# Optimization experiments

Hardware: AMD Instinct MI355X
Metric: run time of the kernel (lower is better)

The kernel has to match this reference:

```python
import jax, jax.numpy as jnp
import numpy as np
from jax import lax

K = 3          # kernel_size
G = 2          # num_groups
DN = ('NHWC', 'HWIO', 'NHWC')


def _conv_same(x, w, b, groups=1):
    y = lax.conv_general_dilated(x, w, (1, 1), 'SAME',
                                 dimension_numbers=DN,
                                 feature_group_count=groups)
    return y + b


def _kernel_grid():
    off = (K - 1) / 2.0
    lin = jnp.linspace(-off, off, K, dtype=jnp.float32)
    dx, dy = jnp.meshgrid(lin, lin)              # 'xy' indexing, like tf default
    return jnp.stack([dx, dy], axis=-1).reshape(K * K, 2)  # [K2, 2] (dx, dy)


def _bilinear_sample(inp, loc):
    # inp: [B,H,W,C], loc: [B,H,W,K2,2] with (x,y) already clipped to valid range
    B, H, W, C = inp.shape
    x, y = loc[..., 0], loc[..., 1]
    x0 = jnp.floor(x); y0 = jnp.floor(y)
    x1 = jnp.clip(x0 + 1.0, 0.0, W - 1.0); x0 = jnp.clip(x0, 0.0, W - 1.0)
    y1 = jnp.clip(y0 + 1.0, 0.0, H - 1.0); y0 = jnp.clip(y0, 0.0, H - 1.0)
    # corner weights (computed from clipped coords, matching the TF code)
    wa = (x1 - x) * (y1 - y)
    wb = (x1 - x) * (y - y0)
    wc = (x - x0) * (y1 - y)
    wd = (x - x0) * (y - y0)
    x0i = x0.astype(jnp.int32); x1i = x1.astype(jnp.int32)
    y0i = y0.astype(jnp.int32); y1i = y1.astype(jnp.int32)
    flat = inp.reshape(B, H * W, C)

    def gather(yi, xi):
        idx = (yi * W + xi).reshape(B, -1, 1)               # [B, H*W*K2, 1]
        v = jnp.take_along_axis(flat, idx, axis=1)          # [B, H*W*K2, C]
        return v.reshape(B, H, W, K * K, C)

    out = (wa[..., None] * gather(y0i, x0i) + wb[..., None] * gather(y1i, x0i)
           + wc[..., None] * gather(y0i, x1i) + wd[..., None] * gather(y1i, x1i))
    return out  # [B,H,W,K2,C]


def _forward(x, off_w, off_b, dw_w, dw_b, pw_w, pw_b):
    B, H, W, C = x.shape
    Cg = C // G
    kg = _kernel_grid()                                     # [K2,2]
    gx, gy = jnp.meshgrid(jnp.arange(W, dtype=jnp.float32),
                          jnp.arange(H, dtype=jnp.float32))
    grid = jnp.stack([gx, gy], axis=-1)                     # [H,W,2] (x,y)
    outs = []
    for g in range(G):
        xi = x[..., g * Cg:(g + 1) * Cg]                    # [B,H,W,Cg]
        offsets = _conv_same(xi, off_w[g], off_b[g])        # [B,H,W,2*K2]
        offsets = offsets.reshape(B, H, W, K * K, 2)
        loc = grid[None, :, :, None, :] + kg[None, None, None] + offsets
        loc = jnp.stack([jnp.clip(loc[..., 0], 0.0, W - 1.0),
                         jnp.clip(loc[..., 1], 0.0, H - 1.0)], axis=-1)
        sampled = _bilinear_sample(xi, loc)                 # [B,H,W,K2,Cg]
        Kin = K * K * Cg
        s = sampled.reshape(B, H, W, Kin)
        s = _conv_same(s, dw_w[g], dw_b[g], groups=Kin)     # depthwise 3x3
        s = _conv_same(s, pw_w[g], pw_b[g])                 # 1x1 pointwise
        outs.append(s)
    return jnp.concatenate(outs, axis=-1)


def setup_inputs() -> dict:
    key = jax.random.key(0)
    ks = jax.random.split(key, 6)
    B, H, W, C = 4, 128, 128, 128
    Cg = C // G
    F = 128
    Fg = F // G
    Kin = K * K * Cg
    x = jax.random.normal(ks[0], (B, H, W, C), jnp.float32)
    # offset conv (zero-init in source; small random weights so offsets ~1px)
    off_w = jax.random.normal(ks[1], (G, K, K, Cg, 2 * K * K), jnp.float32) * 0.05
    off_b = jnp.zeros((G, 2 * K * K), jnp.float32)
    dw_w = jax.random.normal(ks[2], (G, K, K, 1, Kin), jnp.float32) * 0.1
    dw_b = jnp.zeros((G, Kin), jnp.float32)
    pw_w = jax.random.normal(ks[3], (G, 1, 1, Kin, Fg), jnp.float32) / np.sqrt(Kin)
    pw_b = jnp.zeros((G, Fg), jnp.float32)
    return {"x": x, "off_w": off_w, "off_b": off_b,
            "dw_w": dw_w, "dw_b": dw_b, "pw_w": pw_w, "pw_b": pw_b}


def reference(x, off_w, off_b, dw_w, dw_b, pw_w, pw_b):
    return _forward(x, off_w, off_b, dw_w, dw_b, pw_w, pw_b)
```

## Files before the change

kernel.cpp:

```cpp
#include <hip/hip_runtime.h>
#include <hip/hip_bf16.h>

#define HW 128
#define GNUM 2
#define BATCH 4
#define OBT_STRIDE (GNUM * 18 * 2 * 512)
#define PWT_FLOATS 36864
#define OBT_FLOATS 36864

typedef short s16x8 __attribute__((ext_vector_type(8)));
typedef float f32x4 __attribute__((ext_vector_type(4)));

__device__ inline unsigned short f2bf(float f) {
    union { float f; unsigned u; } v;
    v.f = f;
    unsigned r = (v.u + 0x7fffu + ((v.u >> 16) & 1u)) >> 16;
    return (unsigned short)r;
}
__device__ inline unsigned pk2bf(float lo, float hi) {
    __hip_bfloat162 r = __float22bfloat162_rn(float2{lo, hi});
    return *(unsigned*)&r;
}
__device__ inline float blo(unsigned u) {
    union { unsigned u; float f; } v; v.u = u << 16; return v.f;
}
__device__ inline float bhi(unsigned u) {
    union { unsigned u; float f; } v; v.u = u & 0xffff0000u; return v.f;
}

__global__ __launch_bounds__(256) void prep_kernel(
    const float* __restrict__ pw_w, const float* __restrict__ dw_b,
    const float* __restrict__ off_w, unsigned short* __restrict__ pwt,
    unsigned short* __restrict__ obt, float* __restrict__ bias2) {
    const int g = blockIdx.y;
    const int t = threadIdx.x;
    if (blockIdx.x < 9) {
        const int j = blockIdx.x;
        const int wv = t >> 6, lane = t & 63;
        const int f = wv * 16 + (lane & 15);
        const int kbase = (lane >> 4) << 3;
        float part = 0.f;
#pragma unroll
        for (int ks = 0; ks < 2; ++ks)
#pragma unroll
            for (int i = 0; i < 8; ++i) {
                int kin = j * 64 + ks * 32 + kbase + i;
                float v = pw_w[(g * 576 + kin) * 64 + f];
                pwt[((((g * 9 + j) * 4 + wv) * 2 + ks) << 9) + lane * 8 + i] =
                    f2bf(v);
                part += v * dw_b[g * 576 + kin];
            }
        atomicAdd(&bias2[g * 64 + f], part);
    } else {
        const int s = blockIdx.x - 9;
        const int tap = s >> 1;
        for (int e = t; e < 1024; e += 256) {
            int nt = e >> 9, le = e & 511;
            int lane = le >> 3, i = le & 7;
            int k = ((lane >> 4) << 3) + i;
            int c = ((s & 1) << 5) + k;
            int n = (nt << 4) + (lane & 15);
            float v = (n < 18) ? off_w[((g * 9 + tap) * 64 + c) * 18 + n] : 0.f;
            unsigned short hi = f2bf(v);
            unsigned short lo = f2bf(v - blo(hi));
            int idx = (((g * 18 + s) * 2 + nt) << 9) + le;
            obt[idx] = hi;
            obt[OBT_STRIDE + idx] = lo;
        }
    }
}

__global__ __launch_bounds__(256, 4) void deform_fused(
    const float* __restrict__ x, const unsigned short* __restrict__ obt,
    const float* __restrict__ off_b, const float* __restrict__ dw_w,
    const unsigned short* __restrict__ pwt, const float* __restrict__ bias2,
    const float* __restrict__ pw_b, float* __restrict__ out) {
    __shared__ char smem[34016];
    unsigned short* xh = (unsigned short*)smem;
    unsigned short* samp = (unsigned short*)smem;
    unsigned short* dwa = (unsigned short*)(smem + 14400);
    float* offs = (float*)(smem + 23616);
    float4* wlw = (float4*)(smem + 30816);
    int4* wli = (int4*)(smem + 32416);

    const int b = blockIdx.x >> 1, g = blockIdx.x & 1;
    const int tileIdx = blockIdx.y;
    const int h0 = (tileIdx >> 4) << 3, w0 = (tileIdx & 15) << 3;
    const int t = threadIdx.x;
    const int lane = t & 63;
    const int wv = __builtin_amdgcn_readfirstlane(t >> 6);
    const int kq = (lane >> 4) << 3;
    const int col = lane & 15;
    const int rq = (lane >> 4) << 2;

    f32x4 oacc[2][2];
#pragma unroll
    for (int sl = 0; sl < 2; ++sl)
#pragma unroll
        for (int nt = 0; nt < 2; ++nt) oacc[sl][nt] = (f32x4){0.f, 0.f, 0.f, 0.f};
    int mbase[2];
#pragma unroll
    for (int sl = 0; sl < 2; ++sl) {
        int mt = wv + (sl << 2);
        int m = mt * 16 + col;
        if (mt < 7 && m < 100) {
            int opy = m / 10, opx = m - opy * 10;
            mbase[sl] = opy * 12 + opx;
        } else
            mbase[sl] = 0;
    }
    for (int q = 0; q < 2; ++q) {
        if (q) __syncthreads();
        for (int idx = t; idx < 144 * 8; idx += 256) {
            int sp = idx >> 3, cq = idx & 7;
            int sy = sp / 12, sx = sp - sy * 12;
            int gy = h0 - 2 + sy, gx = w0 - 2 + sx;
            uint2 hp = {0, 0}, lp = {0, 0};
            if ((unsigned)gy < HW && (unsigned)gx < HW) {
                const float4 v = *(const float4*)&x[(((b * HW + gy) * HW + gx)
                                                    << 7) +
                                                   (g << 6) + (q << 5) + (cq << 2)];
                hp.x = pk2bf(v.x, v.y);
                hp.y = pk2bf(v.z, v.w);
                lp.x = pk2bf(v.x - blo(hp.x), v.y - bhi(hp.x));
                lp.y = pk2bf(v.z - blo(hp.y), v.w - bhi(hp.y));
            }
            *(uint2*)&xh[sp * 72 + (cq << 2)] = hp;
            *(uint2*)&xh[sp * 72 + 32 + (cq << 2)] = lp;
        }
        __syncthreads();
        for (int tap = 0; tap < 9; ++tap) {
            const int s = (tap << 1) + q;
            const int ky = tap / 3, kx = tap - ky * 3;
            const int shift = ky * 12 + kx;
            const int bidx = ((g * 18 + s) << 1) << 9;
            s16x8 bh0 = *(const s16x8*)&obt[bidx + lane * 8];
            s16x8 bh1 = *(const s16x8*)&obt[bidx + 512 + lane * 8];
            s16x8 bl0 = *(const s16x8*)&obt[OBT_STRIDE + bidx + lane * 8];
            s16x8 bl1 = *(const s16x8*)&obt[OBT_STRIDE + bidx + 512 + lane * 8];
#pragma unroll
            for (int sl = 0; sl < 2; ++sl) {
                if (wv + (sl << 2) < 7) {
                    const int base2 = (mbase[sl] + shift) * 72 + kq;
                    s16x8 ah = *(const s16x8*)&xh[base2];
                    s16x8 al = *(const s16x8*)&xh[base2 + 32];
                    oacc[sl][0] = __builtin_amdgcn_mfma_f32_16x16x32_bf16(
                        ah, bh0, oacc[sl][0], 0, 0, 0);
                    oacc[sl][1] = __builtin_amdgcn_mfma_f32_16x16x32_bf16(
                        ah, bh1, oacc[sl][1], 0, 0, 0);
                    oacc[sl][0] = __builtin_amdgcn_mfma_f32_16x16x32_bf16(
                        al, bh0, oacc[sl][0], 0, 0, 0);
                    oacc[sl][1] = __builtin_amdgcn_mfma_f32_16x16x32_bf16(
                        al, bh1, oacc[sl][1], 0, 0, 0);
                    oacc[sl][0] = __builtin_amdgcn_mfma_f32_16x16x32_bf16(
                        ah, bl0, oacc[sl][0], 0, 0, 0);
                    oacc[sl][1] = __builtin_amdgcn_mfma_f32_16x16x32_bf16(
                        ah, bl1, oacc[sl][1], 0, 0, 0);
                }
            }
        }
    }
#pragma unroll
    for (int sl = 0; sl < 2; ++sl) {
        int mt = wv + (sl << 2);
        if (mt < 7) {
#pragma unroll
            for (int nt = 0; nt < 2; ++nt) {
                int o = (nt << 4) + col;
                if (o < 18) {
                    float ob = off_b[g * 18 + o];
#pragma unroll
                    for (int i = 0; i < 4; ++i) {
                        int m = mt * 16 + rq + i;
                        if (m < 100) offs[m * 18 + o] = oacc[sl][nt][i] + ob;
                    }
                }
            }
        }
    }
    __syncthreads();

    const int fb = wv << 4;
    const int p = lane;
    const int ayp = p >> 3, axp = p & 7;
    const int grp = t >> 4, sl16 = t & 15;

    const float bs = bias2[g * 64 + fb + col] + pw_b[g * 64 + fb + col];
    f32x4 acc[4];
#pragma unroll
    for (int mt = 0; mt < 4; ++mt) acc[mt] = (f32x4){bs, bs, bs, bs};

    for (int j = 0; j < 9; ++j) {
        const int jy = j / 3, jx = j - jy * 3;
        s16x8 bfr[2];
#pragma unroll
        for (int ks = 0; ks < 2; ++ks)
            bfr[ks] = *(const s16x8*)&pwt[((((g * 9 + j) * 4 + wv) * 2 + ks)
                                           << 9) + lane * 8];
        if (t < 100) {
            const int sp = t;
            const int spy = sp / 10, spx = sp - spy * 10;
            const int gy = h0 - 1 + spy, gx = w0 - 1 + spx;
            float4 w4 = {0.f, 0.f, 0.f, 0.f};
            int4 ii = {b << 21, 0, 0, 0};
            if ((unsigned)gy < HW && (unsigned)gx < HW) {
                const float ox = offs[sp * 18 + 2 * j];
                const float oy = offs[sp * 18 + 2 * j + 1];
                float xf = fminf(fmaxf((float)(gx + jx - 1) + ox, 0.f), 127.f);
                float yf = fminf(fmaxf((float)(gy + jy - 1) + oy, 0.f), 127.f);
                float x0 = floorf(xf), y0 = floorf(yf);
                float x1 = fminf(x0 + 1.f, 127.f);
                float y1 = fminf(y0 + 1.f, 127.f);
                w4.x = (x1 - xf) * (y1 - yf);
                w4.y = (x1 - xf) * (yf - y0);
                w4.z = (xf - x0) * (y1 - yf);
                w4.w = (xf - x0) * (yf - y0);
                const int x0i = (int)x0, y0i = (int)y0;
                ii.x = ((b * HW + y0i) * HW + x0i) << 7;
                ii.y = ((int)x1 - x0i) << 7;
                ii.z = ((int)y1 - y0i) << 14;
            }
            wlw[sp] = w4;
            wli[sp] = ii;
        }
        __syncthreads();
        for (int it = 0; it < 7; ++it) {
            const int sp = (it << 4) + grp;
            if (sp < 100) {
                const float4 w4 = wlw[sp];
                const int4 ii = wli[sp];
                const float* xa = x + ii.x + (g << 6) + (sl16 << 2);
                const float4 va = *(const float4*)xa;
                const float4 vb = *(const float4*)(xa + ii.z);
                const float4 vc = *(const float4*)(xa + ii.y);
                const float4 vd = *(const float4*)(xa + ii.y + ii.z);
                float r0 = w4.x * va.x + w4.y * vb.x + w4.z * vc.x + w4.w * vd.x;
                float r1 = w4.x * va.y + w4.y * vb.y + w4.z * vc.y + w4.w * vd.y;
                float r2 = w4.x * va.z + w4.y * vb.z + w4.z * vc.z + w4.w * vd.z;
                float r3 = w4.x * va.w + w4.y * vb.w + w4.z * vc.w + w4.w * vd.w;
                uint2 pk;
                pk.x = pk2bf(r0, r1);
                pk.y = pk2bf(r2, r3);
                *(uint2*)&samp[sp * 72 + (sl16 << 2)] = pk;
            }
        }
        __syncthreads();
#pragma unroll
        for (int cq = 0; cq < 2; ++cq) {
            const int c8 = fb + (cq << 3);
            float d0 = 0.f, d1 = 0.f, d2 = 0.f, d3 = 0.f;
            float d4 = 0.f, d5 = 0.f, d6 = 0.f, d7 = 0.f;
#pragma unroll
            for (int ky = 0; ky < 3; ++ky)
#pragma unroll
                for (int kx = 0; kx < 3; ++kx) {
                    const uint4 hv = *(const uint4*)&samp
                        [((ayp + ky) * 10 + axp + kx) * 72 + c8];
                    const float* wr =
                        &dw_w[((g * 3 + ky) * 3 + kx) * 576 + (j << 6) + c8];
                    d0 += blo(hv.x) * wr[0]; d1 += bhi(hv.x) * wr[1];
                    d2 += blo(hv.y) * wr[2]; d3 += bhi(hv.y) * wr[3];
                    d4 += blo(hv.z) * wr[4]; d5 += bhi(hv.z) * wr[5];
                    d6 += blo(hv.w) * wr[6]; d7 += bhi(hv.w) * wr[7];
                }
            uint4 pk;
            pk.x = pk2bf(d0, d1);
            pk.y = pk2bf(d2, d3);
            pk.z = pk2bf(d4, d5);
            pk.w = pk2bf(d6, d7);
            *(uint4*)&dwa[p * 72 + c8] = pk;
        }
        __syncthreads();
#pragma unroll
        for (int ks = 0; ks < 2; ++ks)
#pragma unroll
            for (int mt = 0; mt < 4; ++mt) {
                s16x8 af = *(const s16x8*)&dwa[(mt * 16 + col) * 72 + ks * 32 +
                                               kq];
                acc[mt] = __builtin_amdgcn_mfma_f32_16x16x32_bf16(
                    af, bfr[ks], acc[mt], 0, 0, 0);
            }
    }
#pragma unroll
    for (int mt = 0; mt < 4; ++mt)
#pragma unroll
        for (int i = 0; i < 4; ++i) {
            int m = mt * 16 + rq + i;
            out[((b * HW + h0 + (m >> 3)) * HW + (w0 + (m & 7))) * 128 +
                (g << 6) + fb + col] = acc[mt][i];
        }
}

extern "C" void kernel_launch(void* const* d_in, const int* in_sizes, int n_in,
                              void* d_out, int out_size, void* d_ws,
                              size_t ws_size, hipStream_t stream) {
    const float* x = (const float*)d_in[0];
    const float* off_w = (const float*)d_in[1];
    const float* off_b = (const float*)d_in[2];
    const float* dw_w = (const float*)d_in[3];
    const float* dw_b = (const float*)d_in[4];
    const float* pw_w = (const float*)d_in[5];
    const float* pw_b = (const float*)d_in[6];

    float* wsf = (float*)d_ws;
    unsigned short* pwt = (unsigned short*)wsf;
    unsigned short* obt = (unsigned short*)(wsf + PWT_FLOATS);
    float* bias2 = wsf + PWT_FLOATS + OBT_FLOATS;

    hipMemsetAsync(bias2, 0, GNUM * 64 * sizeof(float), stream);
    prep_kernel<<<dim3(27, GNUM), dim3(256), 0, stream>>>(pw_w, dw_b, off_w,
                                                          pwt, obt, bias2);
    deform_fused<<<dim3(BATCH * GNUM, 256), dim3(256), 0, stream>>>(
        x, obt, off_b, dw_w, pwt, bias2, pw_b, (float*)d_out);
}
```

Before: 204.9 us.

## Fold depthwise conv weights into pointwise weights and run combined conv on MFMA

```diff
diff --git a/kernel.cpp b/kernel.cpp
--- a/kernel.cpp
+++ b/kernel.cpp
@@ -4,8 +4,8 @@
 #define HW 128
 #define GNUM 2
 #define BATCH 4
+#define W2T_FLOATS 331776
 #define OBT_STRIDE (GNUM * 18 * 2 * 512)
-#define PWT_FLOATS 36864
 #define OBT_FLOATS 36864
 
 typedef short s16x8 __attribute__((ext_vector_type(8)));
@@ -30,8 +30,9 @@
 
 __global__ __launch_bounds__(256) void prep_kernel(
     const float* __restrict__ pw_w, const float* __restrict__ dw_b,
-    const float* __restrict__ off_w, unsigned short* __restrict__ pwt,
-    unsigned short* __restrict__ obt, float* __restrict__ bias2) {
+    const float* __restrict__ off_w, const float* __restrict__ dw_w,
+    unsigned short* __restrict__ w2t, unsigned short* __restrict__ obt,
+    float* __restrict__ bias2) {
     const int g = blockIdx.y;
     const int t = threadIdx.x;
     if (blockIdx.x < 9) {
@@ -39,6 +40,7 @@
         const int wv = t >> 6, lane = t & 63;
         const int f = wv * 16 + (lane & 15);
         const int kbase = (lane >> 4) << 3;
+        float vv[2][8];
         float part = 0.f;
 #pragma unroll
         for (int ks = 0; ks < 2; ++ks)
@@ -46,11 +48,24 @@
             for (int i = 0; i < 8; ++i) {
                 int kin = j * 64 + ks * 32 + kbase + i;
                 float v = pw_w[(g * 576 + kin) * 64 + f];
-                pwt[((((g * 9 + j) * 4 + wv) * 2 + ks) << 9) + lane * 8 + i] =
-                    f2bf(v);
+                vv[ks][i] = v;
                 part += v * dw_b[g * 576 + kin];
             }
         atomicAdd(&bias2[g * 64 + f], part);
+        for (int tap2 = 0; tap2 < 9; ++tap2) {
+#pragma unroll
+            for (int ks = 0; ks < 2; ++ks) {
+                s16x8 w;
+#pragma unroll
+                for (int i = 0; i < 8; ++i) {
+                    int kin = j * 64 + ks * 32 + kbase + i;
+                    w[i] = (short)f2bf(vv[ks][i] *
+                                       dw_w[(g * 9 + tap2) * 576 + kin]);
+                }
+                *(s16x8*)&w2t[(((((g * 9 + j) * 9 + tap2) * 4 + wv) * 2 + ks)
+                               << 9) + lane * 8] = w;
+            }
+        }
     } else {
         const int s = blockIdx.x - 9;
         const int tap = s >> 1;
@@ -72,16 +87,15 @@
 
 __global__ __launch_bounds__(256, 4) void deform_fused(
     const float* __restrict__ x, const unsigned short* __restrict__ obt,
-    const float* __restrict__ off_b, const float* __restrict__ dw_w,
-    const unsigned short* __restrict__ pwt, const float* __restrict__ bias2,
-    const float* __restrict__ pw_b, float* __restrict__ out) {
-    __shared__ char smem[34016];
+    const float* __restrict__ off_b, const unsigned short* __restrict__ w2t,
+    const float* __restrict__ bias2, const float* __restrict__ pw_b,
+    float* __restrict__ out) {
+    __shared__ char smem[31136];
     unsigned short* xh = (unsigned short*)smem;
     unsigned short* samp = (unsigned short*)smem;
-    unsigned short* dwa = (unsigned short*)(smem + 14400);
-    float* offs = (float*)(smem + 23616);
-    float4* wlw = (float4*)(smem + 30816);
-    int4* wli = (int4*)(smem + 32416);
+    float* offs = (float*)(smem + 20736);
+    float4* wlw = (float4*)(smem + 27936);
+    int4* wli = (int4*)(smem + 29536);
 
     const int b = blockIdx.x >> 1, g = blockIdx.x & 1;
     const int tileIdx = blockIdx.y;
@@ -180,23 +194,18 @@
     }
     __syncthreads();
 
-    const int fb = wv << 4;
-    const int p = lane;
-    const int ayp = p >> 3, axp = p & 7;
     const int grp = t >> 4, sl16 = t & 15;
-
-    const float bs = bias2[g * 64 + fb + col] + pw_b[g * 64 + fb + col];
+    const int sbase = ((col >> 3) * 10 + (col & 7)) * 72 + kq;
+    const unsigned short* w2b = w2t + (((g * 9) * 72 + wv * 2) << 9) + lane * 8;
+
+    const float bs = bias2[g * 64 + (wv << 4) + col] +
+                     pw_b[g * 64 + (wv << 4) + col];
     f32x4 acc[4];
 #pragma unroll
     for (int mt = 0; mt < 4; ++mt) acc[mt] = (f32x4){bs, bs, bs, bs};
 
     for (int j = 0; j < 9; ++j) {
         const int jy = j / 3, jx = j - jy * 3;
-        s16x8 bfr[2];
-#pragma unroll
-        for (int ks = 0; ks < 2; ++ks)
-            bfr[ks] = *(const s16x8*)&pwt[((((g * 9 + j) * 4 + wv) * 2 + ks)
-                                           << 9) + lane * 8];
         if (t < 100) {
             const int sp = t;
             const int spy = sp / 10, spx = sp - spy * 10;
@@ -245,42 +254,26 @@
             }
         }
         __syncthreads();
-#pragma unroll
-        for (int cq = 0; cq < 2; ++cq) {
-            const int c8 = fb + (cq << 3);
-            float d0 = 0.f, d1 = 0.f, d2 = 0.f, d3 = 0.f;
-            float d4 = 0.f, d5 = 0.f, d6 = 0.f, d7 = 0.f;
-#pragma unroll
-            for (int ky = 0; ky < 3; ++ky)
-#pragma unroll
-                for (int kx = 0; kx < 3; ++kx) {
-                    const uint4 hv = *(const uint4*)&samp
-                        [((ayp + ky) * 10 + axp + kx) * 72 + c8];
-                    const float* wr =
-                        &dw_w[((g * 3 + ky) * 3 + kx) * 576 + (j << 6) + c8];
-                    d0 += blo(hv.x) * wr[0]; d1 += bhi(hv.x) * wr[1];
-                    d2 += blo(hv.y) * wr[2]; d3 += bhi(hv.y) * wr[3];
-                    d4 += blo(hv.z) * wr[4]; d5 += bhi(hv.z) * wr[5];
-                    d6 += blo(hv.w) * wr[6]; d7 += bhi(hv.w) * wr[7];
-                }
-            uint4 pk;
-            pk.x = pk2bf(d0, d1);
-            pk.y = pk2bf(d2, d3);
-            pk.z = pk2bf(d4, d5);
-            pk.w = pk2bf(d6, d7);
-            *(uint4*)&dwa[p * 72 + c8] = pk;
-        }
-        __syncthreads();
-#pragma unroll
-        for (int ks = 0; ks < 2; ++ks)
+        const unsigned short* w2j = w2b + ((j * 72) << 9);
+#pragma unroll
+        for (int t2 = 0; t2 < 9; ++t2) {
+            const int ky = t2 / 3, kx = t2 - ky * 3;
+            s16x8 b0 = *(const s16x8*)(w2j + ((t2 * 8 + 0) << 9));
+            s16x8 b1 = *(const s16x8*)(w2j + ((t2 * 8 + 1) << 9));
 #pragma unroll
             for (int mt = 0; mt < 4; ++mt) {
-                s16x8 af = *(const s16x8*)&dwa[(mt * 16 + col) * 72 + ks * 32 +
-                                               kq];
+                const unsigned short* ap =
+                    &samp[sbase + (((mt << 1) + ky) * 10 + kx) * 72];
+                s16x8 a0 = *(const s16x8*)ap;
+                s16x8 a1 = *(const s16x8*)(ap + 32);
                 acc[mt] = __builtin_amdgcn_mfma_f32_16x16x32_bf16(
-                    af, bfr[ks], acc[mt], 0, 0, 0);
-            }
-    }
+                    a0, b0, acc[mt], 0, 0, 0);
+                acc[mt] = __builtin_amdgcn_mfma_f32_16x16x32_bf16(
+                    a1, b1, acc[mt], 0, 0, 0);
+            }
+        }
+    }
+    const int fb = wv << 4;
 #pragma unroll
     for (int mt = 0; mt < 4; ++mt)
 #pragma unroll
@@ -303,13 +296,14 @@
     const float* pw_b = (const float*)d_in[6];
 
     float* wsf = (float*)d_ws;
-    unsigned short* pwt = (unsigned short*)wsf;
-    unsigned short* obt = (unsigned short*)(wsf + PWT_FLOATS);
-    float* bias2 = wsf + PWT_FLOATS + OBT_FLOATS;
+    unsigned short* w2t = (unsigned short*)wsf;
+    unsigned short* obt = (unsigned short*)(wsf + W2T_FLOATS);
+    float* bias2 = wsf + W2T_FLOATS + OBT_FLOATS;
 
     hipMemsetAsync(bias2, 0, GNUM * 64 * sizeof(float), stream);
     prep_kernel<<<dim3(27, GNUM), dim3(256), 0, stream>>>(pw_w, dw_b, off_w,
-                                                          pwt, obt, bias2);
+                                                          dw_w, w2t, obt,
+                                                          bias2);
     deform_fused<<<dim3(BATCH * GNUM, 256), dim3(256), 0, stream>>>(
-        x, obt, off_b, dw_w, pwt, bias2, pw_b, (float*)d_out);
-}
+        x, obt, off_b, w2t, bias2, pw_b, (float*)d_out);
+}
```

New measurement: 250.3 us. 1.22x slower.
